# Kernel tuning notes

Measured on AMD Instinct MI355X. Metric: run time of the kernel, lower is better.

Reference implementation:

```python
import jax, jax.numpy as jnp
import numpy as np


def setup_inputs() -> dict:
    key = jax.random.key(0)
    k1, k2, k3, k4 = jax.random.split(key, 4)
    B, N, DIN, DOUT = 4, 4096, 512, 64
    x = jax.random.normal(k1, (B, N, DIN), dtype=jnp.float32)
    Wq = jax.random.normal(k2, (DIN, DOUT), dtype=jnp.float32) * (1.0 / np.sqrt(DIN))
    Wk = jax.random.normal(k3, (DIN, DOUT), dtype=jnp.float32) * (1.0 / np.sqrt(DIN))
    Wv = jax.random.normal(k4, (DIN, DOUT), dtype=jnp.float32) * (1.0 / np.sqrt(DIN))
    return {"x": x, "Wq": Wq, "Wk": Wk, "Wv": Wv}


def reference(x, Wq, Wk, Wv):
    # x: [B, N, Din]; projections: [B, N, Dout]
    q = jnp.einsum('bnd,de->bne', x, Wq)
    k = jnp.einsum('bnd,de->bne', x, Wk)
    v = jnp.einsum('bnd,de->bne', x, Wv)
    N = x.shape[1]
    scale = 1.0 / jnp.sqrt(jnp.asarray(k.shape[-1], dtype=x.dtype))
    # scores: [B, N, N]; causal mask (strict upper triangle -> -inf)
    scores = jnp.einsum('bqe,bke->bqk', q, k)
    causal = jnp.tril(jnp.ones((N, N), dtype=bool))  # True where allowed
    scores = jnp.where(causal[None], scores, -jnp.inf)
    att = jax.nn.softmax(scores * scale, axis=-1)
    # dropout p=0.0 -> identity (eval-mode equivalent)
    return jnp.einsum('bqk,bke->bqe', att, v)
```

## Files before the change

kernel.cpp:

```cpp
#include <hip/hip_runtime.h>
#include <hip/hip_bf16.h>

#define BB 4
#define NN 4096
#define DIN 512
#define DD 64

typedef __attribute__((ext_vector_type(8))) short short8;
typedef __attribute__((ext_vector_type(4))) float f32x4;
typedef __attribute__((ext_vector_type(4))) unsigned short us4;
typedef __attribute__((ext_vector_type(2))) unsigned int u32x2;
using bf16 = __hip_bfloat16;

#define QSCALE 0.18033688011112042f

__device__ inline void mfma_16x16x32(f32x4& d, short8 a, short8 b) {
    asm("v_mfma_f32_16x16x32_bf16 %0, %1, %2, %0" : "+v"(d) : "v"(a), "v"(b));
}

__device__ inline unsigned cvt_pk_bf16(float lo, float hi) {
    unsigned r;
    asm("v_cvt_pk_bf16_f32 %0, %1, %2" : "=v"(r) : "v"(lo), "v"(hi));
    return r;
}

__device__ inline short8 load_cvt8(const float* __restrict__ src) {
    f32x4 f0 = *(const f32x4*)(src);
    f32x4 f1 = *(const f32x4*)(src + 4);
    bf16 t[8];
    #pragma unroll
    for (int j = 0; j < 4; ++j) t[j]     = __float2bfloat16(f0[j]);
    #pragma unroll
    for (int j = 0; j < 4; ++j) t[4 + j] = __float2bfloat16(f1[j]);
    return *(short8*)t;
}

__host__ __device__ inline int pfx(int qt, int cl) {
    int K = 2 << cl;
    int n = qt + K;
    int a = n >> (cl + 1);
    int r = n - (a << (cl + 1));
    return a * (a - 1) * (K >> 1) + r * a;
}

__global__ __launch_bounds__(256) void convw_kernel(
    const float* __restrict__ Wq, const float* __restrict__ Wk,
    const float* __restrict__ Wv, bf16* __restrict__ WT)
{
    int idx = blockIdx.x * 256 + threadIdx.x;
    int w   = idx >> 15;
    int rem = idx & 32767;
    int n   = rem >> 9;
    int kk  = rem & 511;
    const float* W = (w == 0) ? Wq : (w == 1) ? Wk : Wv;
    WT[idx] = __float2bfloat16(W[kk * DD + n]);
}

__global__ __launch_bounds__(256) void proj_kernel(
    const float* __restrict__ x, const bf16* __restrict__ WT,
    bf16* __restrict__ q, bf16* __restrict__ k, bf16* __restrict__ vT)
{
    __shared__ __align__(16) char xs[65536];
    const int tid   = threadIdx.x;
    const int row0  = blockIdx.x * 64;
    const int b     = row0 >> 12;
    const int nrow0 = row0 & 4095;

    const float* xb = x + (size_t)row0 * DIN;
    #pragma unroll
    for (int i = 0; i < 16; ++i) {
        int c   = tid + i * 256;
        int row = c >> 6;
        int cc  = c & 63;
        const float* src = xb + row * DIN + cc * 8;
        int off = row * 1024 + ((cc * 16) ^ ((row & 7) << 4));
        *(short8*)(xs + off) = load_cvt8(src);
    }
    __syncthreads();

    const int lane  = tid & 63;
    const int l16   = lane & 15;
    const int lg    = lane >> 4;
    const int wave  = tid >> 6;
    const int cbase = wave * 48;

    f32x4 acc[4][3];
    #pragma unroll
    for (int rt = 0; rt < 4; ++rt)
        #pragma unroll
        for (int ct = 0; ct < 3; ++ct) acc[rt][ct] = (f32x4){0.f, 0.f, 0.f, 0.f};

    const bf16* wb = WT + (size_t)(cbase + l16) * DIN + lg * 8;

    #pragma unroll 2
    for (int ks = 0; ks < 16; ++ks) {
        short8 a[4], bfr[3];
        #pragma unroll
        for (int rt = 0; rt < 4; ++rt) {
            int row = rt * 16 + l16;
            a[rt] = *(const short8*)(xs + row * 1024 +
                                     ((ks * 64 + lg * 16) ^ ((row & 7) << 4)));
        }
        #pragma unroll
        for (int ct = 0; ct < 3; ++ct)
            bfr[ct] = *(const short8*)(wb + ct * 16 * DIN + ks * 32);
        #pragma unroll
        for (int rt = 0; rt < 4; ++rt)
            #pragma unroll
            for (int ct = 0; ct < 3; ++ct)
                mfma_16x16x32(acc[rt][ct], a[rt], bfr[ct]);
    }

    #pragma unroll
    for (int ct = 0; ct < 3; ++ct) {
        int g = cbase + ct * 16 + l16;
        int w = g >> 6;
        int n = g & 63;
        #pragma unroll
        for (int rt = 0; rt < 4; ++rt) {
            if (w == 2) {
                us4 pv;
                #pragma unroll
                for (int r = 0; r < 4; ++r) {
                    bf16 hv = __float2bfloat16(acc[rt][ct][r]);
                    pv[r] = *(unsigned short*)&hv;
                }
                *(us4*)(vT + ((size_t)b * DD + n) * NN + nrow0 + rt * 16 + lg * 4) = pv;
            } else {
                bf16* dst = (w == 0) ? q : k;
                float sc  = (w == 0) ? QSCALE : 1.0f;
                #pragma unroll
                for (int r = 0; r < 4; ++r) {
                    int row = nrow0 + rt * 16 + lg * 4 + r;
                    dst[((size_t)b * NN + row) * DD + n] =
                        __float2bfloat16(acc[rt][ct][r] * sc);
                }
            }
        }
    }
}

__global__ __launch_bounds__(256) void attn_split_kernel(
    const bf16* __restrict__ q, const bf16* __restrict__ k,
    const bf16* __restrict__ vT,
    unsigned short* __restrict__ partO, float* __restrict__ partML, int cl)
{
    const int perB = pfx(64, cl);
    const int wblk = blockIdx.x;
    const int b    = wblk / perB;
    const int u    = wblk - b * perB;
    int lo = 0, hi = 63;
    while (lo < hi) {
        int mid = (lo + hi + 1) >> 1;
        if (pfx(mid, cl) <= u) lo = mid; else hi = mid - 1;
    }
    const int qt = lo;
    const int s  = u - pfx(qt, cl);
    const size_t sidx = (size_t)wblk;

    const int T  = (qt + 2) >> 1;
    const int t0 = s << cl;
    int t1 = t0 + (1 << cl); if (t1 > T) t1 = T;

    const int wave = threadIdx.x >> 6;
    const int lane = threadIdx.x & 63;
    const int l16  = lane & 15;
    const int lg   = lane >> 4;

    __shared__ __align__(16) char klds[16384];
    __shared__ __align__(16) char vlds[16384];
    __shared__ __align__(16) char plds[4][4096];
    char* pbl = plds[wave];
    const int swz = (l16 & 7) << 4;

    const int row0g = qt * 64 + wave * 16;
    const int qrow  = row0g + l16;

    const bf16* qbase = q + ((size_t)b * NN + row0g + l16) * DD + lg * 8;
    short8 qfrag0 = *(const short8*)(qbase);
    short8 qfrag1 = *(const short8*)(qbase + 32);

    f32x4 oacc[4];
    #pragma unroll
    for (int dt = 0; dt < 4; ++dt) oacc[dt] = (f32x4){0.f, 0.f, 0.f, 0.f};
    float m = -INFINITY, l = 0.f;

    const char* kglob = (const char*)(k  + (size_t)b * NN * DD);
    const char* vglob = (const char*)(vT + (size_t)b * DD * NN);
    short8 kst[4], vst[4];
    int k_wr[4], v_wr[4], v_dd[4];
    #pragma unroll
    for (int i = 0; i < 4; ++i) {
        int L = wave * 4096 + i * 1024 + lane * 16;
        k_wr[i] = L ^ (((L >> 7) & 7) << 4);
        int dd = wave * 16 + i * 4 + (lane >> 4);
        v_dd[i] = dd;
        v_wr[i] = dd * 256 + (((lane & 15) * 16) ^ ((dd & 7) << 4));
    }

    {
        const char* kt = kglob + (size_t)t0 * 16384;
        const char* vt = vglob + (size_t)t0 * 256;
        #pragma unroll
        for (int i = 0; i < 4; ++i)
            kst[i] = *(const short8*)(kt + wave * 4096 + i * 1024 + lane * 16);
        #pragma unroll
        for (int i = 0; i < 4; ++i)
            vst[i] = *(const short8*)(vt + (size_t)v_dd[i] * 8192 + (lane & 15) * 16);
        #pragma unroll
        for (int i = 0; i < 4; ++i) *(short8*)(klds + k_wr[i]) = kst[i];
        #pragma unroll
        for (int i = 0; i < 4; ++i) *(short8*)(vlds + v_wr[i]) = vst[i];
    }
    __syncthreads();

    #pragma unroll 1
    for (int t = t0; t < t1; ++t) {
        f32x4 sc[8];
        #pragma unroll
        for (int ct = 0; ct < 8; ++ct) sc[ct] = (f32x4){0.f, 0.f, 0.f, 0.f};
        __builtin_amdgcn_s_setprio(1);
        #pragma unroll
        for (int ct = 0; ct < 8; ++ct) {
            short8 kf0 = *(const short8*)(klds + (ct * 16 + l16) * 128 + ((lg * 16) ^ swz));
            short8 kf1 = *(const short8*)(klds + (ct * 16 + l16) * 128 + ((64 + lg * 16) ^ swz));
            mfma_16x16x32(sc[ct], kf0, qfrag0);
            mfma_16x16x32(sc[ct], kf1, qfrag1);
        }
        __builtin_amdgcn_s_setprio(0);

        if (t + 1 < t1) {
            const char* kt = kglob + (size_t)(t + 1) * 16384;
            const char* vt = vglob + (size_t)(t + 1) * 256;
            #pragma unroll
            for (int i = 0; i < 4; ++i)
                kst[i] = *(const short8*)(kt + wave * 4096 + i * 1024 + lane * 16);
            #pragma unroll
            for (int i = 0; i < 4; ++i)
                vst[i] = *(const short8*)(vt + (size_t)v_dd[i] * 8192 + (lane & 15) * 16);
        }

        if (t * 128 + 127 > row0g) {
            #pragma unroll
            for (int ct = 0; ct < 8; ++ct) {
                int gk = t * 128 + ct * 16 + lg * 4;
                #pragma unroll
                for (int r = 0; r < 4; ++r)
                    if (gk + r > qrow)
                        sc[ct][r] = -INFINITY;
            }
        }

        float m4[8];
        #pragma unroll
        for (int ct = 0; ct < 8; ++ct)
            m4[ct] = fmaxf(fmaxf(sc[ct][0], sc[ct][1]), fmaxf(sc[ct][2], sc[ct][3]));
        float mt = fmaxf(fmaxf(fmaxf(m4[0], m4[1]), fmaxf(m4[2], m4[3])),
                         fmaxf(fmaxf(m4[4], m4[5]), fmaxf(m4[6], m4[7])));
        mt = fmaxf(mt, __shfl_xor(mt, 16));
        mt = fmaxf(mt, __shfl_xor(mt, 32));

        float mn    = fmaxf(m, mt);
        float alpha = exp2f(m - mn);
        m = mn;

        float s4[8];
        #pragma unroll
        for (int ct = 0; ct < 8; ++ct) {
            float p0 = exp2f(sc[ct][0] - m);
            float p1 = exp2f(sc[ct][1] - m);
            float p2 = exp2f(sc[ct][2] - m);
            float p3 = exp2f(sc[ct][3] - m);
            sc[ct][0] = p0; sc[ct][1] = p1; sc[ct][2] = p2; sc[ct][3] = p3;
            s4[ct] = (p0 + p1) + (p2 + p3);
        }
        float ls = ((s4[0] + s4[1]) + (s4[2] + s4[3])) +
                   ((s4[4] + s4[5]) + (s4[6] + s4[7]));
        ls += __shfl_xor(ls, 16);
        ls += __shfl_xor(ls, 32);
        l = l * alpha + ls;

        float ar[4];
        #pragma unroll
        for (int r = 0; r < 4; ++r) ar[r] = __shfl(alpha, lg * 4 + r);
        #pragma unroll
        for (int dt = 0; dt < 4; ++dt)
            #pragma unroll
            for (int r = 0; r < 4; ++r)
                oacc[dt][r] *= ar[r];

        #pragma unroll
        for (int ct = 0; ct < 8; ++ct) {
            u32x2 pw = (u32x2){cvt_pk_bf16(sc[ct][0], sc[ct][1]),
                               cvt_pk_bf16(sc[ct][2], sc[ct][3])};
            *(u32x2*)(pbl + l16 * 256 + ((ct * 32 + lg * 8) ^ swz)) = pw;
        }
        asm volatile("s_waitcnt lgkmcnt(0)" ::: "memory");
        short8 pa[4];
        #pragma unroll
        for (int kc = 0; kc < 4; ++kc)
            pa[kc] = *(const short8*)(pbl + l16 * 256 + ((kc * 64 + lg * 16) ^ swz));

        __builtin_amdgcn_s_setprio(1);
        #pragma unroll
        for (int dt = 0; dt < 4; ++dt) {
            #pragma unroll
            for (int kc = 0; kc < 4; ++kc) {
                short8 vf = *(const short8*)(vlds + (dt * 16 + l16) * 256 +
                                             ((kc * 64 + lg * 16) ^ swz));
                mfma_16x16x32(oacc[dt], pa[kc], vf);
            }
        }
        __builtin_amdgcn_s_setprio(0);

        if (t + 1 < t1) {
            __syncthreads();
            #pragma unroll
            for (int i = 0; i < 4; ++i) *(short8*)(klds + k_wr[i]) = kst[i];
            #pragma unroll
            for (int i = 0; i < 4; ++i) *(short8*)(vlds + v_wr[i]) = vst[i];
            __syncthreads();
        }
    }

    #pragma unroll
    for (int dt = 0; dt < 4; ++dt)
        #pragma unroll
        for (int r = 0; r < 4; ++r) {
            bf16 hv = __float2bfloat16(oacc[dt][r]);
            partO[sidx * 4096 + wave * 1024 + (dt * 4 + r) * 64 + lane] =
                *(unsigned short*)&hv;
        }
    if (lg == 0) {
        partML[sidx * 128 + wave * 16 + l16]      = m;
        partML[sidx * 128 + 64 + wave * 16 + l16] = l;
    }
}

__global__ __launch_bounds__(256) void combine_kernel(
    const unsigned short* __restrict__ partO, const float* __restrict__ partML,
    float* __restrict__ out, int cl)
{
    const int blk  = blockIdx.x;
    const int qt   = blk & 63;
    const int b    = blk >> 6;
    const int tid  = threadIdx.x;
    const int w    = tid >> 6;
    const int lane = tid & 63;
    const int l16  = lane & 15;
    const int lg   = lane >> 4;

    const int perB = pfx(64, cl);
    const size_t base = (size_t)b * perB + pfx(qt, cl);
    const int K2 = 2 << cl;
    const int U  = (qt + K2) >> (cl + 1);

    float M[4] = {-INFINITY, -INFINITY, -INFINITY, -INFINITY};
    for (int s = 0; s < U; ++s)
        #pragma unroll
        for (int r = 0; r < 4; ++r)
            M[r] = fmaxf(M[r], partML[(base + s) * 128 + w * 16 + lg * 4 + r]);

    float L[4] = {0.f, 0.f, 0.f, 0.f};
    float acc[16];
    #pragma unroll
    for (int i = 0; i < 16; ++i) acc[i] = 0.f;

    for (int s = 0; s < U; ++s) {
        float e[4];
        #pragma unroll
        for (int r = 0; r < 4; ++r) {
            float ms = partML[(base + s) * 128 + w * 16 + lg * 4 + r];
            e[r] = exp2f(ms - M[r]);
            L[r] += partML[(base + s) * 128 + 64 + w * 16 + lg * 4 + r] * e[r];
        }
        #pragma unroll
        for (int reg = 0; reg < 16; ++reg) {
            unsigned fb = ((unsigned)partO[(base + s) * 4096 + w * 1024 + reg * 64 + lane]) << 16;
            acc[reg] += *(float*)&fb * e[reg & 3];
        }
    }
    #pragma unroll
    for (int reg = 0; reg < 16; ++reg) {
        int row = qt * 64 + w * 16 + lg * 4 + (reg & 3);
        int dd  = (reg >> 2) * 16 + l16;
        out[((size_t)b * NN + row) * DD + dd] = acc[reg] / L[reg & 3];
    }
}

extern "C" void kernel_launch(void* const* d_in, const int* in_sizes, int n_in,
                              void* d_out, int out_size, void* d_ws, size_t ws_size,
                              hipStream_t stream) {
    const float* x  = (const float*)d_in[0];
    const float* Wq = (const float*)d_in[1];
    const float* Wk = (const float*)d_in[2];
    const float* Wv = (const float*)d_in[3];

    bf16* q  = (bf16*)d_ws;
    bf16* k  = q  + (size_t)BB * NN * DD;
    bf16* vT = k  + (size_t)BB * NN * DD;
    bf16* WT = vT + (size_t)BB * NN * DD;
    char* pbase = (char*)(WT + 3 * DD * DIN);
    size_t mis = (size_t)pbase & 15;
    if (mis) pbase += 16 - mis;
    size_t fixed = (size_t)(pbase - (char*)d_ws);

    int cl = 1, perB = 0;
    for (; cl <= 3; ++cl) {
        perB = pfx(64, cl);
        size_t need = fixed + (size_t)BB * perB * (128 * 4 + 4096 * 2);
        if (need <= ws_size) break;
    }
    if (cl > 3) { cl = 3; perB = pfx(64, cl); }

    float* partML = (float*)pbase;
    unsigned short* partO = (unsigned short*)(partML + (size_t)BB * perB * 128);

    convw_kernel<<<(3 * DD * DIN) / 256, 256, 0, stream>>>(Wq, Wk, Wv, WT);
    proj_kernel<<<BB * NN / 64, 256, 0, stream>>>(x, WT, q, k, vT);
    attn_split_kernel<<<BB * perB, 256, 0, stream>>>(q, k, vT, partO, partML, cl);
    combine_kernel<<<BB * 64, 256, 0, stream>>>(partO, partML, (float*)d_out, cl);
}
```

Before: 61.29 us.

## Enlarge attention query tile to 128 rows with 8 waves per block

Raises the query tile in the split attention kernel from 64 to 128 rows, using 512 threads (8 waves), so each K/V tile staged in LDS is shared by twice as many query rows. The cooperative K/V load is redistributed across the 512 threads, and the split-count and prefix math, partial buffer strides and combine kernel are adjusted to match. This halves K/V global loads per query row and the number of partials to combine. In exchange there are fewer, larger blocks, which may lower occupancy or balance, and diagonal tiles do more masked work.

```diff
diff --git a/kernel.cpp b/kernel.cpp
--- a/kernel.cpp
+++ b/kernel.cpp
@@ -36,11 +36,10 @@
 }
 
 __host__ __device__ inline int pfx(int qt, int cl) {
-    int K = 2 << cl;
-    int n = qt + K;
-    int a = n >> (cl + 1);
-    int r = n - (a << (cl + 1));
-    return a * (a - 1) * (K >> 1) + r * a;
+    int C = 1 << cl;
+    int a = qt >> cl;
+    int r = qt & (C - 1);
+    return C * a * (a + 1) / 2 + r * (a + 1);
 }
 
 __global__ __launch_bounds__(256) void convw_kernel(
@@ -140,16 +139,16 @@
     }
 }
 
-__global__ __launch_bounds__(256) void attn_split_kernel(
+__global__ __launch_bounds__(512) void attn_split_kernel(
     const bf16* __restrict__ q, const bf16* __restrict__ k,
     const bf16* __restrict__ vT,
     unsigned short* __restrict__ partO, float* __restrict__ partML, int cl)
 {
-    const int perB = pfx(64, cl);
+    const int perB = pfx(32, cl);
     const int wblk = blockIdx.x;
     const int b    = wblk / perB;
     const int u    = wblk - b * perB;
-    int lo = 0, hi = 63;
+    int lo = 0, hi = 31;
     while (lo < hi) {
         int mid = (lo + hi + 1) >> 1;
         if (pfx(mid, cl) <= u) lo = mid; else hi = mid - 1;
@@ -158,22 +157,23 @@
     const int s  = u - pfx(qt, cl);
     const size_t sidx = (size_t)wblk;
 
-    const int T  = (qt + 2) >> 1;
+    const int C  = 1 << cl;
     const int t0 = s << cl;
-    int t1 = t0 + (1 << cl); if (t1 > T) t1 = T;
-
-    const int wave = threadIdx.x >> 6;
-    const int lane = threadIdx.x & 63;
+    int t1 = t0 + C; if (t1 > qt + 1) t1 = qt + 1;
+
+    const int tid  = threadIdx.x;
+    const int wave = tid >> 6;
+    const int lane = tid & 63;
     const int l16  = lane & 15;
     const int lg   = lane >> 4;
 
     __shared__ __align__(16) char klds[16384];
     __shared__ __align__(16) char vlds[16384];
-    __shared__ __align__(16) char plds[4][4096];
+    __shared__ __align__(16) char plds[8][4096];
     char* pbl = plds[wave];
     const int swz = (l16 & 7) << 4;
 
-    const int row0g = qt * 64 + wave * 16;
+    const int row0g = qt * 128 + wave * 16;
     const int qrow  = row0g + l16;
 
     const bf16* qbase = q + ((size_t)b * NN + row0g + l16) * DD + lg * 8;
@@ -187,30 +187,31 @@
 
     const char* kglob = (const char*)(k  + (size_t)b * NN * DD);
     const char* vglob = (const char*)(vT + (size_t)b * DD * NN);
-    short8 kst[4], vst[4];
-    int k_wr[4], v_wr[4], v_dd[4];
-    #pragma unroll
-    for (int i = 0; i < 4; ++i) {
-        int L = wave * 4096 + i * 1024 + lane * 16;
-        k_wr[i] = L ^ (((L >> 7) & 7) << 4);
-        int dd = wave * 16 + i * 4 + (lane >> 4);
-        v_dd[i] = dd;
-        v_wr[i] = dd * 256 + (((lane & 15) * 16) ^ ((dd & 7) << 4));
+    short8 kst[2], vst[2];
+    int k_src[2], k_wr[2], v_src[2], v_wr[2];
+    #pragma unroll
+    for (int i = 0; i < 2; ++i) {
+        int Lk = wave * 2048 + i * 1024 + lane * 16;
+        k_src[i] = Lk;
+        k_wr[i]  = Lk ^ (((Lk >> 7) & 7) << 4);
+        int Lv  = (tid + i * 512) * 16;
+        int dd  = Lv >> 8;
+        int c16 = (Lv >> 4) & 15;
+        v_src[i] = dd * 8192 + c16 * 16;
+        v_wr[i]  = dd * 256 + ((c16 * 16) ^ ((dd & 7) << 4));
     }
 
     {
         const char* kt = kglob + (size_t)t0 * 16384;
         const char* vt = vglob + (size_t)t0 * 256;
         #pragma unroll
-        for (int i = 0; i < 4; ++i)
-            kst[i] = *(const short8*)(kt + wave * 4096 + i * 1024 + lane * 16);
-        #pragma unroll
-        for (int i = 0; i < 4; ++i)
-            vst[i] = *(const short8*)(vt + (size_t)v_dd[i] * 8192 + (lane & 15) * 16);
-        #pragma unroll
-        for (int i = 0; i < 4; ++i) *(short8*)(klds + k_wr[i]) = kst[i];
-        #pragma unroll
-        for (int i = 0; i < 4; ++i) *(short8*)(vlds + v_wr[i]) = vst[i];
+        for (int i = 0; i < 2; ++i) kst[i] = *(const short8*)(kt + k_src[i]);
+        #pragma unroll
+        for (int i = 0; i < 2; ++i) vst[i] = *(const short8*)(vt + v_src[i]);
+        #pragma unroll
+        for (int i = 0; i < 2; ++i) *(short8*)(klds + k_wr[i]) = kst[i];
+        #pragma unroll
+        for (int i = 0; i < 2; ++i) *(short8*)(vlds + v_wr[i]) = vst[i];
     }
     __syncthreads();
 
@@ -233,11 +234,9 @@
             const char* kt = kglob + (size_t)(t + 1) * 16384;
             const char* vt = vglob + (size_t)(t + 1) * 256;
             #pragma unroll
-            for (int i = 0; i < 4; ++i)
-                kst[i] = *(const short8*)(kt + wave * 4096 + i * 1024 + lane * 16);
-            #pragma unroll
-            for (int i = 0; i < 4; ++i)
-                vst[i] = *(const short8*)(vt + (size_t)v_dd[i] * 8192 + (lane & 15) * 16);
+            for (int i = 0; i < 2; ++i) kst[i] = *(const short8*)(kt + k_src[i]);
+            #pragma unroll
+            for (int i = 0; i < 2; ++i) vst[i] = *(const short8*)(vt + v_src[i]);
         }
 
         if (t * 128 + 127 > row0g) {
@@ -316,9 +315,9 @@
         if (t + 1 < t1) {
             __syncthreads();
             #pragma unroll
-            for (int i = 0; i < 4; ++i) *(short8*)(klds + k_wr[i]) = kst[i];
-            #pragma unroll
-            for (int i = 0; i < 4; ++i) *(short8*)(vlds + v_wr[i]) = vst[i];
+            for (int i = 0; i < 2; ++i) *(short8*)(klds + k_wr[i]) = kst[i];
+            #pragma unroll
+            for (int i = 0; i < 2; ++i) *(short8*)(vlds + v_wr[i]) = vst[i];
             __syncthreads();
         }
     }
@@ -328,38 +327,38 @@
         #pragma unroll
         for (int r = 0; r < 4; ++r) {
             bf16 hv = __float2bfloat16(oacc[dt][r]);
-            partO[sidx * 4096 + wave * 1024 + (dt * 4 + r) * 64 + lane] =
+            partO[sidx * 8192 + wave * 1024 + (dt * 4 + r) * 64 + lane] =
                 *(unsigned short*)&hv;
         }
     if (lg == 0) {
-        partML[sidx * 128 + wave * 16 + l16]      = m;
-        partML[sidx * 128 + 64 + wave * 16 + l16] = l;
-    }
-}
-
-__global__ __launch_bounds__(256) void combine_kernel(
+        partML[sidx * 256 + wave * 16 + l16]       = m;
+        partML[sidx * 256 + 128 + wave * 16 + l16] = l;
+    }
+}
+
+__global__ __launch_bounds__(512) void combine_kernel(
     const unsigned short* __restrict__ partO, const float* __restrict__ partML,
     float* __restrict__ out, int cl)
 {
     const int blk  = blockIdx.x;
-    const int qt   = blk & 63;
-    const int b    = blk >> 6;
+    const int qt   = blk & 31;
+    const int b    = blk >> 5;
     const int tid  = threadIdx.x;
     const int w    = tid >> 6;
     const int lane = tid & 63;
     const int l16  = lane & 15;
     const int lg   = lane >> 4;
 
-    const int perB = pfx(64, cl);
+    const int perB = pfx(32, cl);
     const size_t base = (size_t)b * perB + pfx(qt, cl);
-    const int K2 = 2 << cl;
-    const int U  = (qt + K2) >> (cl + 1);
+    const int C = 1 << cl;
+    const int U = (qt + C) >> cl;
 
     float M[4] = {-INFINITY, -INFINITY, -INFINITY, -INFINITY};
     for (int s = 0; s < U; ++s)
         #pragma unroll
         for (int r = 0; r < 4; ++r)
-            M[r] = fmaxf(M[r], partML[(base + s) * 128 + w * 16 + lg * 4 + r]);
+            M[r] = fmaxf(M[r], partML[(base + s) * 256 + w * 16 + lg * 4 + r]);
 
     float L[4] = {0.f, 0.f, 0.f, 0.f};
     float acc[16];
@@ -370,19 +369,19 @@
         float e[4];
         #pragma unroll
         for (int r = 0; r < 4; ++r) {
-            float ms = partML[(base + s) * 128 + w * 16 + lg * 4 + r];
+            float ms = partML[(base + s) * 256 + w * 16 + lg * 4 + r];
             e[r] = exp2f(ms - M[r]);
-            L[r] += partML[(base + s) * 128 + 64 + w * 16 + lg * 4 + r] * e[r];
+            L[r] += partML[(base + s) * 256 + 128 + w * 16 + lg * 4 + r] * e[r];
         }
         #pragma unroll
         for (int reg = 0; reg < 16; ++reg) {
-            unsigned fb = ((unsigned)partO[(base + s) * 4096 + w * 1024 + reg * 64 + lane]) << 16;
+            unsigned fb = ((unsigned)partO[(base + s) * 8192 + w * 1024 + reg * 64 + lane]) << 16;
             acc[reg] += *(float*)&fb * e[reg & 3];
         }
     }
     #pragma unroll
     for (int reg = 0; reg < 16; ++reg) {
-        int row = qt * 64 + w * 16 + lg * 4 + (reg & 3);
+        int row = qt * 128 + w * 16 + lg * 4 + (reg & 3);
         int dd  = (reg >> 2) * 16 + l16;
         out[((size_t)b * NN + row) * DD + dd] = acc[reg] / L[reg & 3];
     }
@@ -406,18 +405,18 @@
     size_t fixed = (size_t)(pbase - (char*)d_ws);
 
     int cl = 1, perB = 0;
-    for (; cl <= 3; ++cl) {
-        perB = pfx(64, cl);
-        size_t need = fixed + (size_t)BB * perB * (128 * 4 + 4096 * 2);
+    for (; cl <= 4; ++cl) {
+        perB = pfx(32, cl);
+        size_t need = fixed + (size_t)BB * perB * (256 * 4 + 8192 * 2);
         if (need <= ws_size) break;
     }
-    if (cl > 3) { cl = 3; perB = pfx(64, cl); }
+    if (cl > 4) { cl = 4; perB = pfx(32, cl); }
 
     float* partML = (float*)pbase;
-    unsigned short* partO = (unsigned short*)(partML + (size_t)BB * perB * 128);
+    unsigned short* partO = (unsigned short*)(partML + (size_t)BB * perB * 256);
 
     convw_kernel<<<(3 * DD * DIN) / 256, 256, 0, stream>>>(Wq, Wk, Wv, WT);
     proj_kernel<<<BB * NN / 64, 256, 0, stream>>>(x, WT, q, k, vT);
-    attn_split_kernel<<<BB * perB, 256, 0, stream>>>(q, k, vT, partO, partML, cl);
-    combine_kernel<<<BB * 64, 256, 0, stream>>>(partO, partML, (float*)d_out, cl);
-}
+    attn_split_kernel<<<BB * perB, 512, 0, stream>>>(q, k, vT, partO, partML, cl);
+    combine_kernel<<<BB * 32, 512, 0, stream>>>(partO, partML, (float*)d_out, cl);
+}
```

New measurement: 67.68 us. +10.4%, slower.
